# Optimization experiments

Measured on AMD Instinct MI355X. Metric: run time of the kernel, lower is better.

Reference implementation:

```python
import jax, jax.numpy as jnp
import numpy as np

B, SRC_LEN, IN_DIM = 4096, 128, 16
H = 64
SEQ_LEN = 100
MEAN_DIM = 4
COV_DIM = MEAN_DIM + MEAN_DIM * (MEAN_DIM - 1) // 2  # 10
SKIP = 4


def _lin_init(key, out_d, in_d):
    k1, k2 = jax.random.split(key)
    bound = 1.0 / np.sqrt(in_d)
    W = jax.random.uniform(k1, (out_d, in_d), minval=-bound, maxval=bound, dtype=jnp.float32)
    b = jax.random.uniform(k2, (out_d,), minval=-bound, maxval=bound, dtype=jnp.float32)
    return W, b


def setup_inputs() -> dict:
    key = jax.random.key(0)
    ks = jax.random.split(key, 16)
    inp = {}
    inp["x"] = jax.random.normal(ks[0], (B, SRC_LEN, IN_DIM), dtype=jnp.float32)
    inp["trg"] = jax.random.normal(ks[1], (B, 1, SKIP), dtype=jnp.float32)
    # encoder GRU (1 layer)
    inp["enc_Wih"], inp["enc_bih"] = _lin_init(ks[2], 3 * H, IN_DIM)
    inp["enc_Whh"], inp["enc_bhh"] = _lin_init(ks[3], 3 * H, H)
    # decoder GRU (1 layer)
    inp["dec_Wih"], inp["dec_bih"] = _lin_init(ks[4], 3 * H, IN_DIM)
    inp["dec_Whh"], inp["dec_bhh"] = _lin_init(ks[5], 3 * H, H)
    # decoder.out: Linear(H -> IN_DIM)
    inp["out_W"], inp["out_b"] = _lin_init(ks[6], IN_DIM, H)
    # initEmbed: Linear(SKIP -> IN_DIM)
    inp["emb_W"], inp["emb_b"] = _lin_init(ks[7], IN_DIM, SKIP)
    # mean head: Linear(IN_DIM->H), GELU, Linear(H->MEAN_DIM)
    inp["mh_W1"], inp["mh_b1"] = _lin_init(ks[8], H, IN_DIM)
    inp["mh_W2"], inp["mh_b2"] = _lin_init(ks[9], MEAN_DIM, H)
    # cov head: Linear(IN_DIM->H), GELU, Linear(H->COV_DIM)
    inp["ch_W1"], inp["ch_b1"] = _lin_init(ks[10], H, IN_DIM)
    inp["ch_W2"], inp["ch_b2"] = _lin_init(ks[11], COV_DIM, H)
    return inp


def _gru_cell(h, xt, Wih, Whh, bih, bhh):
    # PyTorch GRU cell math. h, xt: [B, H], [B, in]
    gi = xt @ Wih.T + bih           # [B, 3H]
    gh = h @ Whh.T + bhh            # [B, 3H]
    i_r, i_z, i_n = jnp.split(gi, 3, axis=-1)
    h_r, h_z, h_n = jnp.split(gh, 3, axis=-1)
    r = jax.nn.sigmoid(i_r + h_r)
    z = jax.nn.sigmoid(i_z + h_z)
    n = jnp.tanh(i_n + r * h_n)
    return (1.0 - z) * n + z * h


def reference(x, trg, enc_Wih, enc_bih, enc_Whh, enc_bhh,
              dec_Wih, dec_bih, dec_Whh, dec_bhh,
              out_W, out_b, emb_W, emb_b,
              mh_W1, mh_b1, mh_W2, mh_b2,
              ch_W1, ch_b1, ch_W2, ch_b2):
    b = x.shape[0]
    # ---- encoder GRU over src_len; only final hidden is used downstream ----
    h0 = jnp.zeros((b, H), dtype=x.dtype)

    def enc_step(h, xt):
        h = _gru_cell(h, xt, enc_Wih, enc_Whh, enc_bih, enc_bhh)
        return h, None

    enc_h, _ = jax.lax.scan(enc_step, h0, jnp.swapaxes(x, 0, 1))

    init_in = trg[:, 0, :] @ emb_W.T + emb_b  # [B, IN_DIM]

    def dec_step(carry, _):
        h, inp = carry
        h = _gru_cell(h, inp, dec_Wih, dec_Whh, dec_bih, dec_bhh)
        o = h @ out_W.T + out_b               # [B, IN_DIM]
        nxt = jax.lax.stop_gradient(o)        # .detach() on fed-back input
        return (h, nxt), o

    (_, _), outs = jax.lax.scan(dec_step, (enc_h, init_in), None, length=SEQ_LEN)
    dec_out = jnp.swapaxes(outs, 0, 1)        # [B, SEQ_LEN, IN_DIM]

    # ---- output heads (Dropout is identity in eval) ----
    means = jax.nn.gelu(dec_out @ mh_W1.T + mh_b1, approximate=False) @ mh_W2.T + mh_b2
    covs = jax.nn.gelu(dec_out @ ch_W1.T + ch_b1, approximate=False) @ ch_W2.T + ch_b2

    inf = jnp.inf
    lower = jnp.array([-inf, -inf, -1.0, -1.0], dtype=means.dtype)
    upper = jnp.array([inf, inf, 1.0, 1.0], dtype=means.dtype)
    means = jnp.maximum(jnp.minimum(means, upper), lower)
    return means, covs
```

## Files before the change

### kernel.cpp

```cpp
#include <hip/hip_runtime.h>
#include <cstdint>
#include <cstddef>

#define BTOT    4096
#define SRCLEN  128
#define INDIM   16
#define HDIM    64
#define SEQLEN  100
#define MEANS_N (BTOT * SEQLEN * 4)

__device__ __forceinline__ float sigmoidf_(float x) {
    return __builtin_amdgcn_rcpf(1.0f + __expf(-x));
}
__device__ __forceinline__ float tanhf_(float x) {
    float e = __expf(2.0f * x);
    return 1.0f - 2.0f * __builtin_amdgcn_rcpf(e + 1.0f);
}
__device__ __forceinline__ float gelu_fast(float x) {
    float z = fabsf(x) * 0.70710678118654752440f;
    float t = __builtin_amdgcn_rcpf(1.0f + 0.3275911f * z);
    float p = t * (0.254829592f +
              t * (-0.284496736f +
              t * (1.421413741f +
              t * (-1.453152027f +
              t * 1.061405429f))));
    float er = 1.0f - p * __expf(-z * z);
    er = copysignf(er, x);
    return 0.5f * x * (1.0f + er);
}

typedef __attribute__((ext_vector_type(8))) short s8v;
typedef __attribute__((ext_vector_type(4))) float f4v;

__device__ __forceinline__ unsigned short f2bf(float x) {
    unsigned u = __float_as_uint(x);
    unsigned r = (u + 0x7FFFu + ((u >> 16) & 1u)) >> 16;
    return (unsigned short)r;
}
__device__ __forceinline__ float bf2f(unsigned short b) {
    return __uint_as_float(((unsigned)b) << 16);
}
__device__ __forceinline__ void split2(float4 a, float4 b, s8v& hi, s8v& lo) {
    float v[8] = {a.x, a.y, a.z, a.w, b.x, b.y, b.z, b.w};
    #pragma unroll
    for (int j = 0; j < 8; ++j) {
        unsigned short h = f2bf(v[j]);
        hi[j] = (short)h;
        lo[j] = (short)f2bf(v[j] - bf2f(h));
    }
}
__device__ __forceinline__ void split8(const float* v, s8v& hi, s8v& lo) {
    #pragma unroll
    for (int j = 0; j < 8; ++j) {
        unsigned short h = f2bf(v[j]);
        hi[j] = (short)h;
        lo[j] = (short)f2bf(v[j] - bf2f(h));
    }
}
__device__ __forceinline__ void load_bfrag(const float* p, s8v& hi, s8v& lo) {
    float4 a = *(const float4*)p;
    float4 b = *(const float4*)(p + 4);
    split2(a, b, hi, lo);
}

typedef __attribute__((ext_vector_type(2))) unsigned int u2v;
__device__ __forceinline__ float half_merge(float own_lo, float send_hi) {
    u2v r = __builtin_amdgcn_permlane32_swap(__float_as_uint(own_lo),
                                             __float_as_uint(send_hi),
                                             false, false);
    return __uint_as_float(r[0]);
}

#define MFMA16(a, b, c) __builtin_amdgcn_mfma_f32_16x16x32_bf16((a), (b), (c), 0, 0, 0)

__global__ __launch_bounds__(256, 2) void enc_mfma_kernel(
    const float* __restrict__ x,
    const float* __restrict__ Wih, const float* __restrict__ bih,
    const float* __restrict__ Whh, const float* __restrict__ bhh,
    float* __restrict__ enc_h)
{
    const int tid  = threadIdx.x;
    const int lane = tid & 63;
    const int w    = tid >> 6;
    const int col  = lane & 15;
    const int q    = lane >> 4;
    const int u    = w * 16 + col;
    const int b0   = blockIdx.x * 8;
    const int rj0  = (q & 1) * 4 + ((q >> 1) << 1);

    __shared__ __align__(16) unsigned short hiL[2][16][72];
    __shared__ __align__(16) unsigned short loL[2][16][72];
    __shared__ __align__(16) unsigned short xhi_l[64][9][16];
    __shared__ __align__(16) unsigned short xlo_l[64][9][16];

    for (int i = tid; i < 2 * 16 * 72; i += 256) {
        ((unsigned short*)hiL)[i] = 0;
        ((unsigned short*)loL)[i] = 0;
    }
    for (int i = tid; i < 64 * 16; i += 256) {
        xhi_l[i >> 4][8][i & 15] = 0;
        xlo_l[i >> 4][8][i & 15] = 0;
    }

    auto stage_x = [&](int c) {
        #pragma unroll
        for (int k = 0; k < 8; ++k) {
            int f   = tid + k * 256;
            int b   = f >> 8;
            int rem = f & 255;
            int tl  = rem >> 2;
            int d4  = (rem & 3) << 2;
            const float* xp = x + ((size_t)(b0 + b) * SRCLEN + (c * 64 + tl)) * INDIM + d4;
            float4 v = *(const float4*)xp;
            float vv[4] = {v.x, v.y, v.z, v.w};
            unsigned short hh[4], ll[4];
            #pragma unroll
            for (int j = 0; j < 4; ++j) {
                hh[j] = f2bf(vv[j]);
                ll[j] = f2bf(vv[j] - bf2f(hh[j]));
            }
            *(ushort4*)&xhi_l[tl][b][d4] = make_ushort4(hh[0], hh[1], hh[2], hh[3]);
            *(ushort4*)&xlo_l[tl][b][d4] = make_ushort4(ll[0], ll[1], ll[2], ll[3]);
        }
    };

    const s8v z8 = {0, 0, 0, 0, 0, 0, 0, 0};
    const f4v z4 = {0.0f, 0.0f, 0.0f, 0.0f};

    s8v brh[3], brl[3], bzh[3], bzl[3], bnhh[2], bnhl[2], bnxh, bnxl;
    load_bfrag(Whh + (size_t)u * 64 + q * 8,              brh[0], brl[0]);
    load_bfrag(Whh + (size_t)u * 64 + 32 + q * 8,         brh[1], brl[1]);
    load_bfrag(Whh + (size_t)(64 + u) * 64 + q * 8,       bzh[0], bzl[0]);
    load_bfrag(Whh + (size_t)(64 + u) * 64 + 32 + q * 8,  bzh[1], bzl[1]);
    load_bfrag(Whh + (size_t)(128 + u) * 64 + q * 8,      bnhh[0], bnhl[0]);
    load_bfrag(Whh + (size_t)(128 + u) * 64 + 32 + q * 8, bnhh[1], bnhl[1]);
    if (q < 2) {
        load_bfrag(Wih + (size_t)u * 16 + q * 8,         brh[2], brl[2]);
        load_bfrag(Wih + (size_t)(64 + u) * 16 + q * 8,  bzh[2], bzl[2]);
        load_bfrag(Wih + (size_t)(128 + u) * 16 + q * 8, bnxh, bnxl);
    } else {
        brh[2] = z8; brl[2] = z8; bzh[2] = z8; bzl[2] = z8; bnxh = z8; bnxl = z8;
    }

    const float br   = bih[u] + bhh[u];
    const float bz   = bih[u + 64] + bhh[u + 64];
    const float bnx  = bih[u + 128];
    const float bnh  = bhh[u + 128];

    const int xb   = (q < 2) ? (col & 7) : 8;
    const int xoff = (q & 1) * 8;
    const unsigned short* xh_base = &xhi_l[0][xb][xoff];
    const unsigned short* xl_base = &xlo_l[0][xb][xoff];

    stage_x(0);
    float hold2[2] = {0.0f, 0.0f};
    __syncthreads();

    int cur = 0;
    for (int t = 0; t < SRCLEN; ++t) {
        if (t == 64) {
            stage_x(1);
            __syncthreads();
        }
        const int tl = t & 63;

        const s8v xh = *(const s8v*)(xh_base + (size_t)tl * 144);
        const s8v xl = *(const s8v*)(xl_base + (size_t)tl * 144);

        const s8v ah0 = *(const s8v*)&hiL[cur][col][q * 8];
        const s8v al0 = *(const s8v*)&loL[cur][col][q * 8];
        const s8v ah1 = *(const s8v*)&hiL[cur][col][32 + q * 8];
        const s8v al1 = *(const s8v*)&loL[cur][col][32 + q * 8];

        f4v accr, accz, accnh, accnx;
        accr  = MFMA16(ah0, brh[0], z4);
        accz  = MFMA16(ah0, bzh[0], z4);
        accnh = MFMA16(ah0, bnhh[0], z4);
        accr  = MFMA16(ah0, brl[0], accr);
        accz  = MFMA16(ah0, bzl[0], accz);
        accnh = MFMA16(ah0, bnhl[0], accnh);
        accr  = MFMA16(al0, brh[0], accr);
        accz  = MFMA16(al0, bzh[0], accz);
        accnh = MFMA16(al0, bnhh[0], accnh);
        accr  = MFMA16(ah1, brh[1], accr);
        accz  = MFMA16(ah1, bzh[1], accz);
        accnh = MFMA16(ah1, bnhh[1], accnh);
        accr  = MFMA16(ah1, brl[1], accr);
        accz  = MFMA16(ah1, bzl[1], accz);
        accnh = MFMA16(ah1, bnhl[1], accnh);
        accr  = MFMA16(al1, brh[1], accr);
        accz  = MFMA16(al1, bzh[1], accz);
        accnh = MFMA16(al1, bnhh[1], accnh);
        accr  = MFMA16(xh, brh[2], accr);
        accz  = MFMA16(xh, bzh[2], accz);
        accnx = MFMA16(xh, bnxh, z4);
        accr  = MFMA16(xh, brl[2], accr);
        accz  = MFMA16(xh, bzl[2], accz);
        accnx = MFMA16(xh, bnxl, accnx);
        accr  = MFMA16(xl, brh[2], accr);
        accz  = MFMA16(xl, bzh[2], accz);
        accnx = MFMA16(xl, bnxh, accnx);

        float pr[2], pz[2], pnh[2], pnx[2];
        pr[0]  = half_merge(accr[0],  accr[2]);
        pr[1]  = half_merge(accr[1],  accr[3]);
        pz[0]  = half_merge(accz[0],  accz[2]);
        pz[1]  = half_merge(accz[1],  accz[3]);
        pnh[0] = half_merge(accnh[0], accnh[2]);
        pnh[1] = half_merge(accnh[1], accnh[3]);
        pnx[0] = half_merge(accnx[0], accnx[2]);
        pnx[1] = half_merge(accnx[1], accnx[3]);

        const int nxt = cur ^ 1;
        #pragma unroll
        for (int j = 0; j < 2; ++j) {
            float r  = sigmoidf_(pr[j] + br);
            float zz = sigmoidf_(pz[j] + bz);
            float n  = tanhf_(pnx[j] + bnx + r * (pnh[j] + bnh));
            float h  = (1.0f - zz) * n + zz * hold2[j];
            hold2[j] = h;
            unsigned short hh = f2bf(h);
            hiL[nxt][rj0 + j][u] = hh;
            loL[nxt][rj0 + j][u] = f2bf(h - bf2f(hh));
        }
        __syncthreads();
        cur ^= 1;
    }

    enc_h[(size_t)(b0 + rj0) * HDIM + u]     = hold2[0];
    enc_h[(size_t)(b0 + rj0 + 1) * HDIM + u] = hold2[1];
}

__global__ __launch_bounds__(256, 2) void dec_mfma_kernel(
    const float* __restrict__ trg,
    const float* __restrict__ Wih, const float* __restrict__ bih,
    const float* __restrict__ Whh, const float* __restrict__ bhh,
    const float* __restrict__ outW, const float* __restrict__ outb,
    const float* __restrict__ embW, const float* __restrict__ embb,
    const float* __restrict__ enc_h,
    float* __restrict__ dec_o)
{
    const int tid  = threadIdx.x;
    const int lane = tid & 63;
    const int w    = tid >> 6;
    const int col  = lane & 15;
    const int q    = lane >> 4;
    const int u    = w * 16 + col;
    const int b0   = blockIdx.x * 8;
    const int rj0  = (q & 1) * 4 + ((q >> 1) << 1);

    __shared__ __align__(16) unsigned short hiL[2][16][72];
    __shared__ __align__(16) unsigned short loL[2][16][72];
    __shared__ float outW_l[16][64];
    __shared__ float init_l[8][16];

    for (int i = tid; i < 16 * 64; i += 256) outW_l[i >> 6][i & 63] = outW[i];
    if (tid < 128) {
        int b = tid >> 4, jj = tid & 15;
        float s = embb[jj];
        #pragma unroll
        for (int s4 = 0; s4 < 4; ++s4)
            s = fmaf(embW[jj * 4 + s4], trg[(size_t)(b0 + b) * 4 + s4], s);
        init_l[b][jj] = s;
    }
    for (int i = tid; i < 2 * 8 * 72; i += 256) {
        int buf = i / (8 * 72);
        int rr  = (i / 72) & 7;
        int cc  = i % 72;
        hiL[buf][8 + rr][cc] = 0;
        loL[buf][8 + rr][cc] = 0;
    }
    if (tid < 128) {
        int idx = tid * 4;
        int bb = idx >> 6, uu = idx & 63;
        float4 v = *(const float4*)(enc_h + (size_t)(b0 + bb) * HDIM + uu);
        float vv[4] = {v.x, v.y, v.z, v.w};
        #pragma unroll
        for (int j = 0; j < 4; ++j) {
            unsigned short hh = f2bf(vv[j]);
            hiL[0][bb][uu + j] = hh;
            loL[0][bb][uu + j] = f2bf(vv[j] - bf2f(hh));
        }
    }
    float hold2[2];
    hold2[0] = enc_h[(size_t)(b0 + rj0) * HDIM + u];
    hold2[1] = enc_h[(size_t)(b0 + rj0 + 1) * HDIM + u];

    __syncthreads();

    const f4v z4 = {0.0f, 0.0f, 0.0f, 0.0f};

    float wh_r[16], wh_z[16], wh_n[16];
    #pragma unroll
    for (int c = 0; c < 2; ++c)
        #pragma unroll
        for (int jj = 0; jj < 8; ++jj) {
            int k = c * 32 + q * 8 + jj;
            wh_r[c * 8 + jj] = Whh[(size_t)u * 64 + k];
            wh_z[c * 8 + jj] = Whh[(size_t)(64 + u) * 64 + k];
            wh_n[c * 8 + jj] = Whh[(size_t)(128 + u) * 64 + k];
        }
    float wi_r[16], wi_z[16], wi_n[16];
    #pragma unroll
    for (int j = 0; j < 16; ++j) {
        wi_r[j] = Wih[(size_t)u * 16 + j];
        wi_z[j] = Wih[(size_t)(64 + u) * 16 + j];
        wi_n[j] = Wih[(size_t)(128 + u) * 16 + j];
    }

    float m_r[16], m_z[16], c_in[16];
    #pragma unroll
    for (int c = 0; c < 2; ++c)
        #pragma unroll
        for (int jj = 0; jj < 8; ++jj) {
            int k = c * 32 + q * 8 + jj;
            float sr = 0.0f, sz = 0.0f, sn = 0.0f;
            #pragma unroll
            for (int j = 0; j < 16; ++j) {
                float ow = outW_l[j][k];
                sr = fmaf(wi_r[j], ow, sr);
                sz = fmaf(wi_z[j], ow, sz);
                sn = fmaf(wi_n[j], ow, sn);
            }
            m_r[c * 8 + jj]  = wh_r[c * 8 + jj] + sr;
            m_z[c * 8 + jj]  = wh_z[c * 8 + jj] + sz;
            c_in[c * 8 + jj] = sn;
        }

    s8v mrh[2], mrl[2], mzh[2], mzl[2], cinh[2], cinl[2], hnh[2], hnl[2];
    split8(m_r,      mrh[0],  mrl[0]);  split8(m_r + 8,  mrh[1],  mrl[1]);
    split8(m_z,      mzh[0],  mzl[0]);  split8(m_z + 8,  mzh[1],  mzl[1]);
    split8(c_in,     cinh[0], cinl[0]); split8(c_in + 8, cinh[1], cinl[1]);
    split8(wh_n,     hnh[0],  hnl[0]);  split8(wh_n + 8, hnh[1],  hnl[1]);
    s8v r0h[2], r0l[2], z0h[2], z0l[2];
    split8(wh_r, r0h[0], r0l[0]); split8(wh_r + 8, r0h[1], r0l[1]);
    split8(wh_z, z0h[0], z0l[0]); split8(wh_z + 8, z0h[1], z0l[1]);
    s8v owh[2], owl[2];
    {
        float ov[16];
        #pragma unroll
        for (int c = 0; c < 2; ++c)
            #pragma unroll
            for (int jj = 0; jj < 8; ++jj)
                ov[c * 8 + jj] = outW_l[col][c * 32 + q * 8 + jj];
        split8(ov, owh[0], owl[0]); split8(ov + 8, owh[1], owl[1]);
    }

    float b_r = bhh[u] + bih[u];
    float b_z = bhh[u + 64] + bih[u + 64];
    float b_in = bih[u + 128];
    const float b_hn = bhh[u + 128];
    #pragma unroll
    for (int j = 0; j < 16; ++j) {
        float obj = outb[j];
        b_r  = fmaf(obj, wi_r[j], b_r);
        b_z  = fmaf(obj, wi_z[j], b_z);
        b_in = fmaf(obj, wi_n[j], b_in);
    }
    const float ob = outb[col];

    float g_r[2], g_z[2], g_n[2];
    #pragma unroll
    for (int j2 = 0; j2 < 2; ++j2) {
        int row = rj0 + j2;
        float sr = bih[u] + bhh[u];
        float sz = bih[u + 64] + bhh[u + 64];
        float sn = bih[u + 128];
        #pragma unroll
        for (int j = 0; j < 16; ++j) {
            float iv = init_l[row][j];
            sr = fmaf(wi_r[j], iv, sr);
            sz = fmaf(wi_z[j], iv, sz);
            sn = fmaf(wi_n[j], iv, sn);
        }
        g_r[j2] = sr; g_z[j2] = sz; g_n[j2] = sn;
    }

    {
        const s8v ah0 = *(const s8v*)&hiL[0][col][q * 8];
        const s8v al0 = *(const s8v*)&loL[0][col][q * 8];
        const s8v ah1 = *(const s8v*)&hiL[0][col][32 + q * 8];
        const s8v al1 = *(const s8v*)&loL[0][col][32 + q * 8];
        f4v ar, az, ahn;
        ar  = MFMA16(ah0, r0h[0], z4);
        az  = MFMA16(ah0, z0h[0], z4);
        ahn = MFMA16(ah0, hnh[0], z4);
        ar  = MFMA16(ah0, r0l[0], ar);
        az  = MFMA16(ah0, z0l[0], az);
        ahn = MFMA16(ah0, hnl[0], ahn);
        ar  = MFMA16(al0, r0h[0], ar);
        az  = MFMA16(al0, z0h[0], az);
        ahn = MFMA16(al0, hnh[0], ahn);
        ar  = MFMA16(ah1, r0h[1], ar);
        az  = MFMA16(ah1, z0h[1], az);
        ahn = MFMA16(ah1, hnh[1], ahn);
        ar  = MFMA16(ah1, r0l[1], ar);
        az  = MFMA16(ah1, z0l[1], az);
        ahn = MFMA16(ah1, hnl[1], ahn);
        ar  = MFMA16(al1, r0h[1], ar);
        az  = MFMA16(al1, z0h[1], az);
        ahn = MFMA16(al1, hnh[1], ahn);

        float pr[2], pz[2], pnh[2];
        pr[0]  = half_merge(ar[0],  ar[2]);
        pr[1]  = half_merge(ar[1],  ar[3]);
        pz[0]  = half_merge(az[0],  az[2]);
        pz[1]  = half_merge(az[1],  az[3]);
        pnh[0] = half_merge(ahn[0], ahn[2]);
        pnh[1] = half_merge(ahn[1], ahn[3]);

        #pragma unroll
        for (int j = 0; j < 2; ++j) {
            float r  = sigmoidf_(pr[j] + g_r[j]);
            float zz = sigmoidf_(pz[j] + g_z[j]);
            float n  = tanhf_(g_n[j] + r * (pnh[j] + b_hn));
            float h  = (1.0f - zz) * n + zz * hold2[j];
            hold2[j] = h;
            unsigned short hh = f2bf(h);
            hiL[1][rj0 + j][u] = hh;
            loL[1][rj0 + j][u] = f2bf(h - bf2f(hh));
        }
        __syncthreads();
    }

    for (int t = 1; t < SEQLEN; ++t) {
        const int cur = t & 1;
        const s8v ah0 = *(const s8v*)&hiL[cur][col][q * 8];
        const s8v al0 = *(const s8v*)&loL[cur][col][q * 8];
        const s8v ah1 = *(const s8v*)&hiL[cur][col][32 + q * 8];
        const s8v al1 = *(const s8v*)&loL[cur][col][32 + q * 8];

        if (w == ((t - 1) & 3)) {
            f4v oa;
            oa = MFMA16(ah0, owh[0], z4);
            oa = MFMA16(ah0, owl[0], oa);
            oa = MFMA16(al0, owh[0], oa);
            oa = MFMA16(ah1, owh[1], oa);
            oa = MFMA16(ah1, owl[1], oa);
            oa = MFMA16(al1, owh[1], oa);
            if (q < 2) {
                #pragma unroll
                for (int i = 0; i < 4; ++i)
                    dec_o[(((size_t)(b0 + q * 4 + i) * SEQLEN) + (t - 1)) * INDIM + col] = oa[i] + ob;
            }
        }

        f4v ar, az, ain, ahn;
        ar  = MFMA16(ah0, mrh[0], z4);
        az  = MFMA16(ah0, mzh[0], z4);
        ain = MFMA16(ah0, cinh[0], z4);
        ahn = MFMA16(ah0, hnh[0], z4);
        ar  = MFMA16(ah0, mrl[0], ar);
        az  = MFMA16(ah0, mzl[0], az);
        ain = MFMA16(ah0, cinl[0], ain);
        ahn = MFMA16(ah0, hnl[0], ahn);
        ar  = MFMA16(al0, mrh[0], ar);
        az  = MFMA16(al0, mzh[0], az);
        ain = MFMA16(al0, cinh[0], ain);
        ahn = MFMA16(al0, hnh[0], ahn);
        ar  = MFMA16(ah1, mrh[1], ar);
        az  = MFMA16(ah1, mzh[1], az);
        ain = MFMA16(ah1, cinh[1], ain);
        ahn = MFMA16(ah1, hnh[1], ahn);
        ar  = MFMA16(ah1, mrl[1], ar);
        az  = MFMA16(ah1, mzl[1], az);
        ain = MFMA16(ah1, cinl[1], ain);
        ahn = MFMA16(ah1, hnl[1], ahn);
        ar  = MFMA16(al1, mrh[1], ar);
        az  = MFMA16(al1, mzh[1], az);
        ain = MFMA16(al1, cinh[1], ain);
        ahn = MFMA16(al1, hnh[1], ahn);

        float pr[2], pz[2], pin[2], pnh[2];
        pr[0]  = half_merge(ar[0],  ar[2]);
        pr[1]  = half_merge(ar[1],  ar[3]);
        pz[0]  = half_merge(az[0],  az[2]);
        pz[1]  = half_merge(az[1],  az[3]);
        pin[0] = half_merge(ain[0], ain[2]);
        pin[1] = half_merge(ain[1], ain[3]);
        pnh[0] = half_merge(ahn[0], ahn[2]);
        pnh[1] = half_merge(ahn[1], ahn[3]);

        const int nxt = cur ^ 1;
        #pragma unroll
        for (int j = 0; j < 2; ++j) {
            float r  = sigmoidf_(pr[j] + b_r);
            float zz = sigmoidf_(pz[j] + b_z);
            float n  = tanhf_(pin[j] + b_in + r * (pnh[j] + b_hn));
            float h  = (1.0f - zz) * n + zz * hold2[j];
            hold2[j] = h;
            unsigned short hh = f2bf(h);
            hiL[nxt][rj0 + j][u] = hh;
            loL[nxt][rj0 + j][u] = f2bf(h - bf2f(hh));
        }
        __syncthreads();
    }

    if (w == 0) {
        const s8v ah0 = *(const s8v*)&hiL[0][col][q * 8];
        const s8v al0 = *(const s8v*)&loL[0][col][q * 8];
        const s8v ah1 = *(const s8v*)&hiL[0][col][32 + q * 8];
        const s8v al1 = *(const s8v*)&loL[0][col][32 + q * 8];
        f4v oa;
        oa = MFMA16(ah0, owh[0], z4);
        oa = MFMA16(ah0, owl[0], oa);
        oa = MFMA16(al0, owh[0], oa);
        oa = MFMA16(ah1, owh[1], oa);
        oa = MFMA16(ah1, owl[1], oa);
        oa = MFMA16(al1, owh[1], oa);
        if (q < 2) {
            #pragma unroll
            for (int i = 0; i < 4; ++i)
                dec_o[(((size_t)(b0 + q * 4 + i) * SEQLEN) + (SEQLEN - 1)) * INDIM + col] = oa[i] + ob;
        }
    }
}

__global__ __launch_bounds__(256) void heads_kernel(
    const float* __restrict__ dec_o,
    const float* __restrict__ mW1, const float* __restrict__ mb1,
    const float* __restrict__ mW2, const float* __restrict__ mb2,
    const float* __restrict__ cW1, const float* __restrict__ cb1,
    const float* __restrict__ cW2, const float* __restrict__ cb2,
    float* __restrict__ out)
{
    const int tid = threadIdx.x;

    __shared__ __align__(16) float lW1m[64][16];
    __shared__ __align__(16) float lW1c[64][16];
    __shared__ __align__(16) float lW2t[64][16];

    for (int i = tid; i < 1024; i += 256) {
        lW1m[i >> 4][i & 15] = mW1[i];
        lW1c[i >> 4][i & 15] = cW1[i];
    }
    if (tid < 64) {
        #pragma unroll
        for (int j = 0; j < 4; ++j)  lW2t[tid][j]     = mW2[j * 64 + tid];
        #pragma unroll
        for (int j = 0; j < 10; ++j) lW2t[tid][4 + j] = cW2[j * 64 + tid];
        lW2t[tid][14] = mb1[tid];
        lW2t[tid][15] = cb1[tid];
    }
    __syncthreads();

    const size_t rbase = (size_t)blockIdx.x * 1024 + tid;

    float o[4][16];
    #pragma unroll
    for (int k = 0; k < 4; ++k) {
        const float4* op = (const float4*)(dec_o + (rbase + (size_t)k * 256) * 16);
        #pragma unroll
        for (int c = 0; c < 4; ++c) {
            float4 v = op[c];
            o[k][4 * c + 0] = v.x; o[k][4 * c + 1] = v.y;
            o[k][4 * c + 2] = v.z; o[k][4 * c + 3] = v.w;
        }
    }

    float m[4][4], cv[4][10];
    {
        float mb2v[4], cb2v[10];
        #pragma unroll
        for (int j = 0; j < 4; ++j)  mb2v[j] = mb2[j];
        #pragma unroll
        for (int j = 0; j < 10; ++j) cb2v[j] = cb2[j];
        #pragma unroll
        for (int k = 0; k < 4; ++k) {
            #pragma unroll
            for (int j = 0; j < 4; ++j)  m[k][j]  = mb2v[j];
            #pragma unroll
            for (int j = 0; j < 10; ++j) cv[k][j] = cb2v[j];
        }
    }

    #pragma unroll 2
    for (int hu = 0; hu < 64; ++hu) {
        const float4 a0 = *(const float4*)&lW1m[hu][0];
        const float4 a1 = *(const float4*)&lW1m[hu][4];
        const float4 a2 = *(const float4*)&lW1m[hu][8];
        const float4 a3 = *(const float4*)&lW1m[hu][12];
        const float4 c0 = *(const float4*)&lW1c[hu][0];
        const float4 c1 = *(const float4*)&lW1c[hu][4];
        const float4 c2 = *(const float4*)&lW1c[hu][8];
        const float4 c3 = *(const float4*)&lW1c[hu][12];
        const float4 t0 = *(const float4*)&lW2t[hu][0];
        const float4 t1 = *(const float4*)&lW2t[hu][4];
        const float4 t2 = *(const float4*)&lW2t[hu][8];
        const float4 t3 = *(const float4*)&lW2t[hu][12];

        #pragma unroll
        for (int k = 0; k < 4; ++k) {
            float hm = t3.z;
            hm = fmaf(a0.x, o[k][0],  hm); hm = fmaf(a0.y, o[k][1],  hm);
            hm = fmaf(a0.z, o[k][2],  hm); hm = fmaf(a0.w, o[k][3],  hm);
            hm = fmaf(a1.x, o[k][4],  hm); hm = fmaf(a1.y, o[k][5],  hm);
            hm = fmaf(a1.z, o[k][6],  hm); hm = fmaf(a1.w, o[k][7],  hm);
            hm = fmaf(a2.x, o[k][8],  hm); hm = fmaf(a2.y, o[k][9],  hm);
            hm = fmaf(a2.z, o[k][10], hm); hm = fmaf(a2.w, o[k][11], hm);
            hm = fmaf(a3.x, o[k][12], hm); hm = fmaf(a3.y, o[k][13], hm);
            hm = fmaf(a3.z, o[k][14], hm); hm = fmaf(a3.w, o[k][15], hm);
            float gm = gelu_fast(hm);
            m[k][0] = fmaf(t0.x, gm, m[k][0]); m[k][1] = fmaf(t0.y, gm, m[k][1]);
            m[k][2] = fmaf(t0.z, gm, m[k][2]); m[k][3] = fmaf(t0.w, gm, m[k][3]);

            float hc = t3.w;
            hc = fmaf(c0.x, o[k][0],  hc); hc = fmaf(c0.y, o[k][1],  hc);
            hc = fmaf(c0.z, o[k][2],  hc); hc = fmaf(c0.w, o[k][3],  hc);
            hc = fmaf(c1.x, o[k][4],  hc); hc = fmaf(c1.y, o[k][5],  hc);
            hc = fmaf(c1.z, o[k][6],  hc); hc = fmaf(c1.w, o[k][7],  hc);
            hc = fmaf(c2.x, o[k][8],  hc); hc = fmaf(c2.y, o[k][9],  hc);
            hc = fmaf(c2.z, o[k][10], hc); hc = fmaf(c2.w, o[k][11], hc);
            hc = fmaf(c3.x, o[k][12], hc); hc = fmaf(c3.y, o[k][13], hc);
            hc = fmaf(c3.z, o[k][14], hc); hc = fmaf(c3.w, o[k][15], hc);
            float gc = gelu_fast(hc);
            cv[k][0] = fmaf(t1.x, gc, cv[k][0]); cv[k][1] = fmaf(t1.y, gc, cv[k][1]);
            cv[k][2] = fmaf(t1.z, gc, cv[k][2]); cv[k][3] = fmaf(t1.w, gc, cv[k][3]);
            cv[k][4] = fmaf(t2.x, gc, cv[k][4]); cv[k][5] = fmaf(t2.y, gc, cv[k][5]);
            cv[k][6] = fmaf(t2.z, gc, cv[k][6]); cv[k][7] = fmaf(t2.w, gc, cv[k][7]);
            cv[k][8] = fmaf(t3.x, gc, cv[k][8]); cv[k][9] = fmaf(t3.y, gc, cv[k][9]);
        }
    }

    float* means = out;
    float* covs  = out + MEANS_N;
    #pragma unroll
    for (int k = 0; k < 4; ++k) {
        const size_t r = rbase + (size_t)k * 256;
        m[k][2] = fminf(fmaxf(m[k][2], -1.0f), 1.0f);
        m[k][3] = fminf(fmaxf(m[k][3], -1.0f), 1.0f);
        #pragma unroll
        for (int j = 0; j < 4; ++j)  means[r * 4 + j] = m[k][j];
        #pragma unroll
        for (int j = 0; j < 10; ++j) covs[r * 10 + j] = cv[k][j];
    }
}

extern "C" void kernel_launch(void* const* d_in, const int* in_sizes, int n_in,
                              void* d_out, int out_size, void* d_ws, size_t ws_size,
                              hipStream_t stream)
{
    const float* x    = (const float*)d_in[0];
    const float* trg  = (const float*)d_in[1];
    const float* eWih = (const float*)d_in[2];
    const float* ebih = (const float*)d_in[3];
    const float* eWhh = (const float*)d_in[4];
    const float* ebhh = (const float*)d_in[5];
    const float* dWih = (const float*)d_in[6];
    const float* dbih = (const float*)d_in[7];
    const float* dWhh = (const float*)d_in[8];
    const float* dbhh = (const float*)d_in[9];
    const float* outW = (const float*)d_in[10];
    const float* outb = (const float*)d_in[11];
    const float* embW = (const float*)d_in[12];
    const float* embb = (const float*)d_in[13];
    const float* mW1  = (const float*)d_in[14];
    const float* mb1  = (const float*)d_in[15];
    const float* mW2  = (const float*)d_in[16];
    const float* mb2  = (const float*)d_in[17];
    const float* cW1  = (const float*)d_in[18];
    const float* cb1  = (const float*)d_in[19];
    const float* cW2  = (const float*)d_in[20];
    const float* cb2  = (const float*)d_in[21];

    float* ws    = (float*)d_ws;
    float* enc_h = ws;
    float* dec_o = ws + (size_t)BTOT * HDIM;
    float* outp  = (float*)d_out;

    enc_mfma_kernel<<<dim3(BTOT / 8), dim3(256), 0, stream>>>(x, eWih, ebih, eWhh, ebhh, enc_h);
    dec_mfma_kernel<<<dim3(BTOT / 8), dim3(256), 0, stream>>>(trg, dWih, dbih, dWhh, dbhh,
                                                              outW, outb, embW, embb, enc_h, dec_o);
    heads_kernel<<<dim3((BTOT * SEQLEN) / 1024), dim3(256), 0, stream>>>(
        dec_o, mW1, mb1, mW2, mb2, cW1, cb1, cW2, cb2, outp);
}
```

Baseline: 374.8 us.

## Fuse encoder and decoder GRU kernels and halve rows per heads thread

Merges the encoder and decoder GRU kernels into one kernel, so the encoder's final hidden state passes directly in registers and LDS instead of through a global workspace round-trip and a second launch. The decoder weight setup now follows the encoder loop in the same block. The heads kernel is also changed to process 2 rows per thread instead of 4, doubling its grid. The trade-offs are higher register and LDS pressure in the fused kernel, which could reduce occupancy, and less per-thread reuse of head weights.

```diff
diff --git a/kernel.cpp b/kernel.cpp
--- a/kernel.cpp
+++ b/kernel.cpp
@@ -73,11 +73,16 @@
 
 #define MFMA16(a, b, c) __builtin_amdgcn_mfma_f32_16x16x32_bf16((a), (b), (c), 0, 0, 0)
 
-__global__ __launch_bounds__(256, 2) void enc_mfma_kernel(
+__global__ __launch_bounds__(256, 2) void fused_gru_kernel(
     const float* __restrict__ x,
-    const float* __restrict__ Wih, const float* __restrict__ bih,
-    const float* __restrict__ Whh, const float* __restrict__ bhh,
-    float* __restrict__ enc_h)
+    const float* __restrict__ eWih, const float* __restrict__ ebih,
+    const float* __restrict__ eWhh, const float* __restrict__ ebhh,
+    const float* __restrict__ dWih, const float* __restrict__ dbih,
+    const float* __restrict__ dWhh, const float* __restrict__ dbhh,
+    const float* __restrict__ outW, const float* __restrict__ outb,
+    const float* __restrict__ embW, const float* __restrict__ embb,
+    const float* __restrict__ trg,
+    float* __restrict__ dec_o)
 {
     const int tid  = threadIdx.x;
     const int lane = tid & 63;
@@ -92,6 +97,18 @@
     __shared__ __align__(16) unsigned short loL[2][16][72];
     __shared__ __align__(16) unsigned short xhi_l[64][9][16];
     __shared__ __align__(16) unsigned short xlo_l[64][9][16];
+    __shared__ float outW_l[16][64];
+    __shared__ float init_l[8][16];
+
+    for (int i = tid; i < 16 * 64; i += 256) outW_l[i >> 6][i & 63] = outW[i];
+    if (tid < 128) {
+        int b = tid >> 4, jj = tid & 15;
+        float s = embb[jj];
+        #pragma unroll
+        for (int s4 = 0; s4 < 4; ++s4)
+            s = fmaf(embW[jj * 4 + s4], trg[(size_t)(b0 + b) * 4 + s4], s);
+        init_l[b][jj] = s;
+    }
 
     for (int i = tid; i < 2 * 16 * 72; i += 256) {
         ((unsigned short*)hiL)[i] = 0;
@@ -127,310 +144,320 @@
     const s8v z8 = {0, 0, 0, 0, 0, 0, 0, 0};
     const f4v z4 = {0.0f, 0.0f, 0.0f, 0.0f};
 
-    s8v brh[3], brl[3], bzh[3], bzl[3], bnhh[2], bnhl[2], bnxh, bnxl;
-    load_bfrag(Whh + (size_t)u * 64 + q * 8,              brh[0], brl[0]);
-    load_bfrag(Whh + (size_t)u * 64 + 32 + q * 8,         brh[1], brl[1]);
-    load_bfrag(Whh + (size_t)(64 + u) * 64 + q * 8,       bzh[0], bzl[0]);
-    load_bfrag(Whh + (size_t)(64 + u) * 64 + 32 + q * 8,  bzh[1], bzl[1]);
-    load_bfrag(Whh + (size_t)(128 + u) * 64 + q * 8,      bnhh[0], bnhl[0]);
-    load_bfrag(Whh + (size_t)(128 + u) * 64 + 32 + q * 8, bnhh[1], bnhl[1]);
-    if (q < 2) {
-        load_bfrag(Wih + (size_t)u * 16 + q * 8,         brh[2], brl[2]);
-        load_bfrag(Wih + (size_t)(64 + u) * 16 + q * 8,  bzh[2], bzl[2]);
-        load_bfrag(Wih + (size_t)(128 + u) * 16 + q * 8, bnxh, bnxl);
-    } else {
-        brh[2] = z8; brl[2] = z8; bzh[2] = z8; bzl[2] = z8; bnxh = z8; bnxl = z8;
-    }
-
-    const float br   = bih[u] + bhh[u];
-    const float bz   = bih[u + 64] + bhh[u + 64];
-    const float bnx  = bih[u + 128];
-    const float bnh  = bhh[u + 128];
-
-    const int xb   = (q < 2) ? (col & 7) : 8;
-    const int xoff = (q & 1) * 8;
-    const unsigned short* xh_base = &xhi_l[0][xb][xoff];
-    const unsigned short* xl_base = &xlo_l[0][xb][xoff];
-
-    stage_x(0);
-    float hold2[2] = {0.0f, 0.0f};
-    __syncthreads();
-
-    int cur = 0;
-    for (int t = 0; t < SRCLEN; ++t) {
-        if (t == 64) {
-            stage_x(1);
+    {
+        s8v brh[3], brl[3], bzh[3], bzl[3], bnhh[2], bnhl[2], bnxh, bnxl;
+        load_bfrag(eWhh + (size_t)u * 64 + q * 8,              brh[0], brl[0]);
+        load_bfrag(eWhh + (size_t)u * 64 + 32 + q * 8,         brh[1], brl[1]);
+        load_bfrag(eWhh + (size_t)(64 + u) * 64 + q * 8,       bzh[0], bzl[0]);
+        load_bfrag(eWhh + (size_t)(64 + u) * 64 + 32 + q * 8,  bzh[1], bzl[1]);
+        load_bfrag(eWhh + (size_t)(128 + u) * 64 + q * 8,      bnhh[0], bnhl[0]);
+        load_bfrag(eWhh + (size_t)(128 + u) * 64 + 32 + q * 8, bnhh[1], bnhl[1]);
+        if (q < 2) {
+            load_bfrag(eWih + (size_t)u * 16 + q * 8,         brh[2], brl[2]);
+            load_bfrag(eWih + (size_t)(64 + u) * 16 + q * 8,  bzh[2], bzl[2]);
+            load_bfrag(eWih + (size_t)(128 + u) * 16 + q * 8, bnxh, bnxl);
+        } else {
+            brh[2] = z8; brl[2] = z8; bzh[2] = z8; bzl[2] = z8; bnxh = z8; bnxl = z8;
+        }
+
+        const float br   = ebih[u] + ebhh[u];
+        const float bz   = ebih[u + 64] + ebhh[u + 64];
+        const float bnx  = ebih[u + 128];
+        const float bnh  = ebhh[u + 128];
+
+        const int xb   = (q < 2) ? (col & 7) : 8;
+        const int xoff = (q & 1) * 8;
+        const unsigned short* xh_base = &xhi_l[0][xb][xoff];
+        const unsigned short* xl_base = &xlo_l[0][xb][xoff];
+
+        stage_x(0);
+        float hold2e[2] = {0.0f, 0.0f};
+        __syncthreads();
+
+        int cur = 0;
+        for (int t = 0; t < SRCLEN; ++t) {
+            if (t == 64) {
+                stage_x(1);
+                __syncthreads();
+            }
+            const int tl = t & 63;
+
+            const s8v xh = *(const s8v*)(xh_base + (size_t)tl * 144);
+            const s8v xl = *(const s8v*)(xl_base + (size_t)tl * 144);
+
+            const s8v ah0 = *(const s8v*)&hiL[cur][col][q * 8];
+            const s8v al0 = *(const s8v*)&loL[cur][col][q * 8];
+            const s8v ah1 = *(const s8v*)&hiL[cur][col][32 + q * 8];
+            const s8v al1 = *(const s8v*)&loL[cur][col][32 + q * 8];
+
+            f4v accr, accz, accnh, accnx;
+            accr  = MFMA16(ah0, brh[0], z4);
+            accz  = MFMA16(ah0, bzh[0], z4);
+            accnh = MFMA16(ah0, bnhh[0], z4);
+            accr  = MFMA16(ah0, brl[0], accr);
+            accz  = MFMA16(ah0, bzl[0], accz);
+            accnh = MFMA16(ah0, bnhl[0], accnh);
+            accr  = MFMA16(al0, brh[0], accr);
+            accz  = MFMA16(al0, bzh[0], accz);
+            accnh = MFMA16(al0, bnhh[0], accnh);
+            accr  = MFMA16(ah1, brh[1], accr);
+            accz  = MFMA16(ah1, bzh[1], accz);
+            accnh = MFMA16(ah1, bnhh[1], accnh);
+            accr  = MFMA16(ah1, brl[1], accr);
+            accz  = MFMA16(ah1, bzl[1], accz);
+            accnh = MFMA16(ah1, bnhl[1], accnh);
+            accr  = MFMA16(al1, brh[1], accr);
+            accz  = MFMA16(al1, bzh[1], accz);
+            accnh = MFMA16(al1, bnhh[1], accnh);
+            accr  = MFMA16(xh, brh[2], accr);
+            accz  = MFMA16(xh, bzh[2], accz);
+            accnx = MFMA16(xh, bnxh, z4);
+            accr  = MFMA16(xh, brl[2], accr);
+            accz  = MFMA16(xh, bzl[2], accz);
+            accnx = MFMA16(xh, bnxl, accnx);
+            accr  = MFMA16(xl, brh[2], accr);
+            accz  = MFMA16(xl, bzh[2], accz);
+            accnx = MFMA16(xl, bnxh, accnx);
+
+            float pr[2], pz[2], pnh[2], pnx[2];
+            pr[0]  = half_merge(accr[0],  accr[2]);
+            pr[1]  = half_merge(accr[1],  accr[3]);
+            pz[0]  = half_merge(accz[0],  accz[2]);
+            pz[1]  = half_merge(accz[1],  accz[3]);
+            pnh[0] = half_merge(accnh[0], accnh[2]);
+            pnh[1] = half_merge(accnh[1], accnh[3]);
+            pnx[0] = half_merge(accnx[0], accnx[2]);
+            pnx[1] = half_merge(accnx[1], accnx[3]);
+
+            const int nxt = cur ^ 1;
+            #pragma unroll
+            for (int j = 0; j < 2; ++j) {
+                float r  = sigmoidf_(pr[j] + br);
+                float zz = sigmoidf_(pz[j] + bz);
+                float n  = tanhf_(pnx[j] + bnx + r * (pnh[j] + bnh));
+                float h  = (1.0f - zz) * n + zz * hold2e[j];
+                hold2e[j] = h;
+                unsigned short hh = f2bf(h);
+                hiL[nxt][rj0 + j][u] = hh;
+                loL[nxt][rj0 + j][u] = f2bf(h - bf2f(hh));
+            }
             __syncthreads();
-        }
-        const int tl = t & 63;
-
-        const s8v xh = *(const s8v*)(xh_base + (size_t)tl * 144);
-        const s8v xl = *(const s8v*)(xl_base + (size_t)tl * 144);
-
-        const s8v ah0 = *(const s8v*)&hiL[cur][col][q * 8];
-        const s8v al0 = *(const s8v*)&loL[cur][col][q * 8];
-        const s8v ah1 = *(const s8v*)&hiL[cur][col][32 + q * 8];
-        const s8v al1 = *(const s8v*)&loL[cur][col][32 + q * 8];
-
-        f4v accr, accz, accnh, accnx;
-        accr  = MFMA16(ah0, brh[0], z4);
-        accz  = MFMA16(ah0, bzh[0], z4);
-        accnh = MFMA16(ah0, bnhh[0], z4);
-        accr  = MFMA16(ah0, brl[0], accr);
-        accz  = MFMA16(ah0, bzl[0], accz);
-        accnh = MFMA16(ah0, bnhl[0], accnh);
-        accr  = MFMA16(al0, brh[0], accr);
-        accz  = MFMA16(al0, bzh[0], accz);
-        accnh = MFMA16(al0, bnhh[0], accnh);
-        accr  = MFMA16(ah1, brh[1], accr);
-        accz  = MFMA16(ah1, bzh[1], accz);
-        accnh = MFMA16(ah1, bnhh[1], accnh);
-        accr  = MFMA16(ah1, brl[1], accr);
-        accz  = MFMA16(ah1, bzl[1], accz);
-        accnh = MFMA16(ah1, bnhl[1], accnh);
-        accr  = MFMA16(al1, brh[1], accr);
-        accz  = MFMA16(al1, bzh[1], accz);
-        accnh = MFMA16(al1, bnhh[1], accnh);
-        accr  = MFMA16(xh, brh[2], accr);
-        accz  = MFMA16(xh, bzh[2], accz);
-        accnx = MFMA16(xh, bnxh, z4);
-        accr  = MFMA16(xh, brl[2], accr);
-        accz  = MFMA16(xh, bzl[2], accz);
-        accnx = MFMA16(xh, bnxl, accnx);
-        accr  = MFMA16(xl, brh[2], accr);
-        accz  = MFMA16(xl, bzh[2], accz);
-        accnx = MFMA16(xl, bnxh, accnx);
-
-        float pr[2], pz[2], pnh[2], pnx[2];
-        pr[0]  = half_merge(accr[0],  accr[2]);
-        pr[1]  = half_merge(accr[1],  accr[3]);
-        pz[0]  = half_merge(accz[0],  accz[2]);
-        pz[1]  = half_merge(accz[1],  accz[3]);
-        pnh[0] = half_merge(accnh[0], accnh[2]);
-        pnh[1] = half_merge(accnh[1], accnh[3]);
-        pnx[0] = half_merge(accnx[0], accnx[2]);
-        pnx[1] = half_merge(accnx[1], accnx[3]);
-
-        const int nxt = cur ^ 1;
-        #pragma unroll
-        for (int j = 0; j < 2; ++j) {
-            float r  = sigmoidf_(pr[j] + br);
-            float zz = sigmoidf_(pz[j] + bz);
-            float n  = tanhf_(pnx[j] + bnx + r * (pnh[j] + bnh));
-            float h  = (1.0f - zz) * n + zz * hold2[j];
-            hold2[j] = h;
-            unsigned short hh = f2bf(h);
-            hiL[nxt][rj0 + j][u] = hh;
-            loL[nxt][rj0 + j][u] = f2bf(h - bf2f(hh));
-        }
-        __syncthreads();
-        cur ^= 1;
-    }
-
-    enc_h[(size_t)(b0 + rj0) * HDIM + u]     = hold2[0];
-    enc_h[(size_t)(b0 + rj0 + 1) * HDIM + u] = hold2[1];
-}
-
-__global__ __launch_bounds__(256, 2) void dec_mfma_kernel(
-    const float* __restrict__ trg,
-    const float* __restrict__ Wih, const float* __restrict__ bih,
-    const float* __restrict__ Whh, const float* __restrict__ bhh,
-    const float* __restrict__ outW, const float* __restrict__ outb,
-    const float* __restrict__ embW, const float* __restrict__ embb,
-    const float* __restrict__ enc_h,
-    float* __restrict__ dec_o)
-{
-    const int tid  = threadIdx.x;
-    const int lane = tid & 63;
-    const int w    = tid >> 6;
-    const int col  = lane & 15;
-    const int q    = lane >> 4;
-    const int u    = w * 16 + col;
-    const int b0   = blockIdx.x * 8;
-    const int rj0  = (q & 1) * 4 + ((q >> 1) << 1);
-
-    __shared__ __align__(16) unsigned short hiL[2][16][72];
-    __shared__ __align__(16) unsigned short loL[2][16][72];
-    __shared__ float outW_l[16][64];
-    __shared__ float init_l[8][16];
-
-    for (int i = tid; i < 16 * 64; i += 256) outW_l[i >> 6][i & 63] = outW[i];
-    if (tid < 128) {
-        int b = tid >> 4, jj = tid & 15;
-        float s = embb[jj];
-        #pragma unroll
-        for (int s4 = 0; s4 < 4; ++s4)
-            s = fmaf(embW[jj * 4 + s4], trg[(size_t)(b0 + b) * 4 + s4], s);
-        init_l[b][jj] = s;
-    }
-    for (int i = tid; i < 2 * 8 * 72; i += 256) {
-        int buf = i / (8 * 72);
-        int rr  = (i / 72) & 7;
-        int cc  = i % 72;
-        hiL[buf][8 + rr][cc] = 0;
-        loL[buf][8 + rr][cc] = 0;
-    }
-    if (tid < 128) {
-        int idx = tid * 4;
-        int bb = idx >> 6, uu = idx & 63;
-        float4 v = *(const float4*)(enc_h + (size_t)(b0 + bb) * HDIM + uu);
-        float vv[4] = {v.x, v.y, v.z, v.w};
-        #pragma unroll
-        for (int j = 0; j < 4; ++j) {
-            unsigned short hh = f2bf(vv[j]);
-            hiL[0][bb][uu + j] = hh;
-            loL[0][bb][uu + j] = f2bf(vv[j] - bf2f(hh));
-        }
-    }
-    float hold2[2];
-    hold2[0] = enc_h[(size_t)(b0 + rj0) * HDIM + u];
-    hold2[1] = enc_h[(size_t)(b0 + rj0 + 1) * HDIM + u];
-
-    __syncthreads();
-
-    const f4v z4 = {0.0f, 0.0f, 0.0f, 0.0f};
-
-    float wh_r[16], wh_z[16], wh_n[16];
-    #pragma unroll
-    for (int c = 0; c < 2; ++c)
-        #pragma unroll
-        for (int jj = 0; jj < 8; ++jj) {
-            int k = c * 32 + q * 8 + jj;
-            wh_r[c * 8 + jj] = Whh[(size_t)u * 64 + k];
-            wh_z[c * 8 + jj] = Whh[(size_t)(64 + u) * 64 + k];
-            wh_n[c * 8 + jj] = Whh[(size_t)(128 + u) * 64 + k];
-        }
-    float wi_r[16], wi_z[16], wi_n[16];
-    #pragma unroll
-    for (int j = 0; j < 16; ++j) {
-        wi_r[j] = Wih[(size_t)u * 16 + j];
-        wi_z[j] = Wih[(size_t)(64 + u) * 16 + j];
-        wi_n[j] = Wih[(size_t)(128 + u) * 16 + j];
-    }
-
-    float m_r[16], m_z[16], c_in[16];
-    #pragma unroll
-    for (int c = 0; c < 2; ++c)
-        #pragma unroll
-        for (int jj = 0; jj < 8; ++jj) {
-            int k = c * 32 + q * 8 + jj;
-            float sr = 0.0f, sz = 0.0f, sn = 0.0f;
+            cur ^= 1;
+        }
+
+        float hold2[2] = {hold2e[0], hold2e[1]};
+
+        float wh_r[16], wh_z[16], wh_n[16];
+        #pragma unroll
+        for (int c = 0; c < 2; ++c)
+            #pragma unroll
+            for (int jj = 0; jj < 8; ++jj) {
+                int k = c * 32 + q * 8 + jj;
+                wh_r[c * 8 + jj] = dWhh[(size_t)u * 64 + k];
+                wh_z[c * 8 + jj] = dWhh[(size_t)(64 + u) * 64 + k];
+                wh_n[c * 8 + jj] = dWhh[(size_t)(128 + u) * 64 + k];
+            }
+        float wi_r[16], wi_z[16], wi_n[16];
+        #pragma unroll
+        for (int j = 0; j < 16; ++j) {
+            wi_r[j] = dWih[(size_t)u * 16 + j];
+            wi_z[j] = dWih[(size_t)(64 + u) * 16 + j];
+            wi_n[j] = dWih[(size_t)(128 + u) * 16 + j];
+        }
+
+        float m_r[16], m_z[16], c_in[16];
+        #pragma unroll
+        for (int c = 0; c < 2; ++c)
+            #pragma unroll
+            for (int jj = 0; jj < 8; ++jj) {
+                int k = c * 32 + q * 8 + jj;
+                float sr = 0.0f, sz = 0.0f, sn = 0.0f;
+                #pragma unroll
+                for (int j = 0; j < 16; ++j) {
+                    float ow = outW_l[j][k];
+                    sr = fmaf(wi_r[j], ow, sr);
+                    sz = fmaf(wi_z[j], ow, sz);
+                    sn = fmaf(wi_n[j], ow, sn);
+                }
+                m_r[c * 8 + jj]  = wh_r[c * 8 + jj] + sr;
+                m_z[c * 8 + jj]  = wh_z[c * 8 + jj] + sz;
+                c_in[c * 8 + jj] = sn;
+            }
+
+        s8v mrh[2], mrl[2], mzh[2], mzl[2], cinh[2], cinl[2], hnh[2], hnl[2];
+        split8(m_r,      mrh[0],  mrl[0]);  split8(m_r + 8,  mrh[1],  mrl[1]);
+        split8(m_z,      mzh[0],  mzl[0]);  split8(m_z + 8,  mzh[1],  mzl[1]);
+        split8(c_in,     cinh[0], cinl[0]); split8(c_in + 8, cinh[1], cinl[1]);
+        split8(wh_n,     hnh[0],  hnl[0]);  split8(wh_n + 8, hnh[1],  hnl[1]);
+        s8v r0h[2], r0l[2], z0h[2], z0l[2];
+        split8(wh_r, r0h[0], r0l[0]); split8(wh_r + 8, r0h[1], r0l[1]);
+        split8(wh_z, z0h[0], z0l[0]); split8(wh_z + 8, z0h[1], z0l[1]);
+        s8v owh[2], owl[2];
+        {
+            float ov[16];
+            #pragma unroll
+            for (int c = 0; c < 2; ++c)
+                #pragma unroll
+                for (int jj = 0; jj < 8; ++jj)
+                    ov[c * 8 + jj] = outW_l[col][c * 32 + q * 8 + jj];
+            split8(ov, owh[0], owl[0]); split8(ov + 8, owh[1], owl[1]);
+        }
+
+        float b_r = dbhh[u] + dbih[u];
+        float b_z = dbhh[u + 64] + dbih[u + 64];
+        float b_in = dbih[u + 128];
+        const float b_hn = dbhh[u + 128];
+        #pragma unroll
+        for (int j = 0; j < 16; ++j) {
+            float obj = outb[j];
+            b_r  = fmaf(obj, wi_r[j], b_r);
+            b_z  = fmaf(obj, wi_z[j], b_z);
+            b_in = fmaf(obj, wi_n[j], b_in);
+        }
+        const float ob = outb[col];
+
+        float g_r[2], g_z[2], g_n[2];
+        #pragma unroll
+        for (int j2 = 0; j2 < 2; ++j2) {
+            int row = rj0 + j2;
+            float sr = dbih[u] + dbhh[u];
+            float sz = dbih[u + 64] + dbhh[u + 64];
+            float sn = dbih[u + 128];
             #pragma unroll
             for (int j = 0; j < 16; ++j) {
-                float ow = outW_l[j][k];
-                sr = fmaf(wi_r[j], ow, sr);
-                sz = fmaf(wi_z[j], ow, sz);
-                sn = fmaf(wi_n[j], ow, sn);
-            }
-            m_r[c * 8 + jj]  = wh_r[c * 8 + jj] + sr;
-            m_z[c * 8 + jj]  = wh_z[c * 8 + jj] + sz;
-            c_in[c * 8 + jj] = sn;
-        }
-
-    s8v mrh[2], mrl[2], mzh[2], mzl[2], cinh[2], cinl[2], hnh[2], hnl[2];
-    split8(m_r,      mrh[0],  mrl[0]);  split8(m_r + 8,  mrh[1],  mrl[1]);
-    split8(m_z,      mzh[0],  mzl[0]);  split8(m_z + 8,  mzh[1],  mzl[1]);
-    split8(c_in,     cinh[0], cinl[0]); split8(c_in + 8, cinh[1], cinl[1]);
-    split8(wh_n,     hnh[0],  hnl[0]);  split8(wh_n + 8, hnh[1],  hnl[1]);
-    s8v r0h[2], r0l[2], z0h[2], z0l[2];
-    split8(wh_r, r0h[0], r0l[0]); split8(wh_r + 8, r0h[1], r0l[1]);
-    split8(wh_z, z0h[0], z0l[0]); split8(wh_z + 8, z0h[1], z0l[1]);
-    s8v owh[2], owl[2];
-    {
-        float ov[16];
-        #pragma unroll
-        for (int c = 0; c < 2; ++c)
-            #pragma unroll
-            for (int jj = 0; jj < 8; ++jj)
-                ov[c * 8 + jj] = outW_l[col][c * 32 + q * 8 + jj];
-        split8(ov, owh[0], owl[0]); split8(ov + 8, owh[1], owl[1]);
-    }
-
-    float b_r = bhh[u] + bih[u];
-    float b_z = bhh[u + 64] + bih[u + 64];
-    float b_in = bih[u + 128];
-    const float b_hn = bhh[u + 128];
-    #pragma unroll
-    for (int j = 0; j < 16; ++j) {
-        float obj = outb[j];
-        b_r  = fmaf(obj, wi_r[j], b_r);
-        b_z  = fmaf(obj, wi_z[j], b_z);
-        b_in = fmaf(obj, wi_n[j], b_in);
-    }
-    const float ob = outb[col];
-
-    float g_r[2], g_z[2], g_n[2];
-    #pragma unroll
-    for (int j2 = 0; j2 < 2; ++j2) {
-        int row = rj0 + j2;
-        float sr = bih[u] + bhh[u];
-        float sz = bih[u + 64] + bhh[u + 64];
-        float sn = bih[u + 128];
-        #pragma unroll
-        for (int j = 0; j < 16; ++j) {
-            float iv = init_l[row][j];
-            sr = fmaf(wi_r[j], iv, sr);
-            sz = fmaf(wi_z[j], iv, sz);
-            sn = fmaf(wi_n[j], iv, sn);
-        }
-        g_r[j2] = sr; g_z[j2] = sz; g_n[j2] = sn;
-    }
-
-    {
-        const s8v ah0 = *(const s8v*)&hiL[0][col][q * 8];
-        const s8v al0 = *(const s8v*)&loL[0][col][q * 8];
-        const s8v ah1 = *(const s8v*)&hiL[0][col][32 + q * 8];
-        const s8v al1 = *(const s8v*)&loL[0][col][32 + q * 8];
-        f4v ar, az, ahn;
-        ar  = MFMA16(ah0, r0h[0], z4);
-        az  = MFMA16(ah0, z0h[0], z4);
-        ahn = MFMA16(ah0, hnh[0], z4);
-        ar  = MFMA16(ah0, r0l[0], ar);
-        az  = MFMA16(ah0, z0l[0], az);
-        ahn = MFMA16(ah0, hnl[0], ahn);
-        ar  = MFMA16(al0, r0h[0], ar);
-        az  = MFMA16(al0, z0h[0], az);
-        ahn = MFMA16(al0, hnh[0], ahn);
-        ar  = MFMA16(ah1, r0h[1], ar);
-        az  = MFMA16(ah1, z0h[1], az);
-        ahn = MFMA16(ah1, hnh[1], ahn);
-        ar  = MFMA16(ah1, r0l[1], ar);
-        az  = MFMA16(ah1, z0l[1], az);
-        ahn = MFMA16(ah1, hnl[1], ahn);
-        ar  = MFMA16(al1, r0h[1], ar);
-        az  = MFMA16(al1, z0h[1], az);
-        ahn = MFMA16(al1, hnh[1], ahn);
-
-        float pr[2], pz[2], pnh[2];
-        pr[0]  = half_merge(ar[0],  ar[2]);
-        pr[1]  = half_merge(ar[1],  ar[3]);
-        pz[0]  = half_merge(az[0],  az[2]);
-        pz[1]  = half_merge(az[1],  az[3]);
-        pnh[0] = half_merge(ahn[0], ahn[2]);
-        pnh[1] = half_merge(ahn[1], ahn[3]);
-
-        #pragma unroll
-        for (int j = 0; j < 2; ++j) {
-            float r  = sigmoidf_(pr[j] + g_r[j]);
-            float zz = sigmoidf_(pz[j] + g_z[j]);
-            float n  = tanhf_(g_n[j] + r * (pnh[j] + b_hn));
-            float h  = (1.0f - zz) * n + zz * hold2[j];
-            hold2[j] = h;
-            unsigned short hh = f2bf(h);
-            hiL[1][rj0 + j][u] = hh;
-            loL[1][rj0 + j][u] = f2bf(h - bf2f(hh));
-        }
-        __syncthreads();
-    }
-
-    for (int t = 1; t < SEQLEN; ++t) {
-        const int cur = t & 1;
-        const s8v ah0 = *(const s8v*)&hiL[cur][col][q * 8];
-        const s8v al0 = *(const s8v*)&loL[cur][col][q * 8];
-        const s8v ah1 = *(const s8v*)&hiL[cur][col][32 + q * 8];
-        const s8v al1 = *(const s8v*)&loL[cur][col][32 + q * 8];
-
-        if (w == ((t - 1) & 3)) {
+                float iv = init_l[row][j];
+                sr = fmaf(wi_r[j], iv, sr);
+                sz = fmaf(wi_z[j], iv, sz);
+                sn = fmaf(wi_n[j], iv, sn);
+            }
+            g_r[j2] = sr; g_z[j2] = sz; g_n[j2] = sn;
+        }
+
+        {
+            const s8v ah0 = *(const s8v*)&hiL[0][col][q * 8];
+            const s8v al0 = *(const s8v*)&loL[0][col][q * 8];
+            const s8v ah1 = *(const s8v*)&hiL[0][col][32 + q * 8];
+            const s8v al1 = *(const s8v*)&loL[0][col][32 + q * 8];
+            f4v ar, az, ahn;
+            ar  = MFMA16(ah0, r0h[0], z4);
+            az  = MFMA16(ah0, z0h[0], z4);
+            ahn = MFMA16(ah0, hnh[0], z4);
+            ar  = MFMA16(ah0, r0l[0], ar);
+            az  = MFMA16(ah0, z0l[0], az);
+            ahn = MFMA16(ah0, hnl[0], ahn);
+            ar  = MFMA16(al0, r0h[0], ar);
+            az  = MFMA16(al0, z0h[0], az);
+            ahn = MFMA16(al0, hnh[0], ahn);
+            ar  = MFMA16(ah1, r0h[1], ar);
+            az  = MFMA16(ah1, z0h[1], az);
+            ahn = MFMA16(ah1, hnh[1], ahn);
+            ar  = MFMA16(ah1, r0l[1], ar);
+            az  = MFMA16(ah1, z0l[1], az);
+            ahn = MFMA16(ah1, hnl[1], ahn);
+            ar  = MFMA16(al1, r0h[1], ar);
+            az  = MFMA16(al1, z0h[1], az);
+            ahn = MFMA16(al1, hnh[1], ahn);
+
+            float pr[2], pz[2], pnh[2];
+            pr[0]  = half_merge(ar[0],  ar[2]);
+            pr[1]  = half_merge(ar[1],  ar[3]);
+            pz[0]  = half_merge(az[0],  az[2]);
+            pz[1]  = half_merge(az[1],  az[3]);
+            pnh[0] = half_merge(ahn[0], ahn[2]);
+            pnh[1] = half_merge(ahn[1], ahn[3]);
+
+            #pragma unroll
+            for (int j = 0; j < 2; ++j) {
+                float r  = sigmoidf_(pr[j] + g_r[j]);
+                float zz = sigmoidf_(pz[j] + g_z[j]);
+                float n  = tanhf_(g_n[j] + r * (pnh[j] + b_hn));
+                float h  = (1.0f - zz) * n + zz * hold2[j];
+                hold2[j] = h;
+                unsigned short hh = f2bf(h);
+                hiL[1][rj0 + j][u] = hh;
+                loL[1][rj0 + j][u] = f2bf(h - bf2f(hh));
+            }
+            __syncthreads();
+        }
+
+        for (int t = 1; t < SEQLEN; ++t) {
+            const int dcur = t & 1;
+            const s8v ah0 = *(const s8v*)&hiL[dcur][col][q * 8];
+            const s8v al0 = *(const s8v*)&loL[dcur][col][q * 8];
+            const s8v ah1 = *(const s8v*)&hiL[dcur][col][32 + q * 8];
+            const s8v al1 = *(const s8v*)&loL[dcur][col][32 + q * 8];
+
+            if (w == ((t - 1) & 3)) {
+                f4v oa;
+                oa = MFMA16(ah0, owh[0], z4);
+                oa = MFMA16(ah0, owl[0], oa);
+                oa = MFMA16(al0, owh[0], oa);
+                oa = MFMA16(ah1, owh[1], oa);
+                oa = MFMA16(ah1, owl[1], oa);
+                oa = MFMA16(al1, owh[1], oa);
+                if (q < 2) {
+                    #pragma unroll
+                    for (int i = 0; i < 4; ++i)
+                        dec_o[(((size_t)(b0 + q * 4 + i) * SEQLEN) + (t - 1)) * INDIM + col] = oa[i] + ob;
+                }
+            }
+
+            f4v ar, az, ain, ahn;
+            ar  = MFMA16(ah0, mrh[0], z4);
+            az  = MFMA16(ah0, mzh[0], z4);
+            ain = MFMA16(ah0, cinh[0], z4);
+            ahn = MFMA16(ah0, hnh[0], z4);
+            ar  = MFMA16(ah0, mrl[0], ar);
+            az  = MFMA16(ah0, mzl[0], az);
+            ain = MFMA16(ah0, cinl[0], ain);
+            ahn = MFMA16(ah0, hnl[0], ahn);
+            ar  = MFMA16(al0, mrh[0], ar);
+            az  = MFMA16(al0, mzh[0], az);
+            ain = MFMA16(al0, cinh[0], ain);
+            ahn = MFMA16(al0, hnh[0], ahn);
+            ar  = MFMA16(ah1, mrh[1], ar);
+            az  = MFMA16(ah1, mzh[1], az);
+            ain = MFMA16(ah1, cinh[1], ain);
+            ahn = MFMA16(ah1, hnh[1], ahn);
+            ar  = MFMA16(ah1, mrl[1], ar);
+            az  = MFMA16(ah1, mzl[1], az);
+            ain = MFMA16(ah1, cinl[1], ain);
+            ahn = MFMA16(ah1, hnl[1], ahn);
+            ar  = MFMA16(al1, mrh[1], ar);
+            az  = MFMA16(al1, mzh[1], az);
+            ain = MFMA16(al1, cinh[1], ain);
+            ahn = MFMA16(al1, hnh[1], ahn);
+
+            float pr[2], pz[2], pin[2], pnh[2];
+            pr[0]  = half_merge(ar[0],  ar[2]);
+            pr[1]  = half_merge(ar[1],  ar[3]);
+            pz[0]  = half_merge(az[0],  az[2]);
+            pz[1]  = half_merge(az[1],  az[3]);
+            pin[0] = half_merge(ain[0], ain[2]);
+            pin[1] = half_merge(ain[1], ain[3]);
+            pnh[0] = half_merge(ahn[0], ahn[2]);
+            pnh[1] = half_merge(ahn[1], ahn[3]);
+
+            const int nxt = dcur ^ 1;
+            #pragma unroll
+            for (int j = 0; j < 2; ++j) {
+                float r  = sigmoidf_(pr[j] + b_r);
+                float zz = sigmoidf_(pz[j] + b_z);
+                float n  = tanhf_(pin[j] + b_in + r * (pnh[j] + b_hn));
+                float h  = (1.0f - zz) * n + zz * hold2[j];
+                hold2[j] = h;
+                unsigned short hh = f2bf(h);
+                hiL[nxt][rj0 + j][u] = hh;
+                loL[nxt][rj0 + j][u] = f2bf(h - bf2f(hh));
+            }
+            __syncthreads();
+        }
+
+        if (w == 0) {
+            const s8v ah0 = *(const s8v*)&hiL[0][col][q * 8];
+            const s8v al0 = *(const s8v*)&loL[0][col][q * 8];
+            const s8v ah1 = *(const s8v*)&hiL[0][col][32 + q * 8];
+            const s8v al1 = *(const s8v*)&loL[0][col][32 + q * 8];
             f4v oa;
             oa = MFMA16(ah0, owh[0], z4);
             oa = MFMA16(ah0, owl[0], oa);
@@ -441,77 +468,8 @@
             if (q < 2) {
                 #pragma unroll
                 for (int i = 0; i < 4; ++i)
-                    dec_o[(((size_t)(b0 + q * 4 + i) * SEQLEN) + (t - 1)) * INDIM + col] = oa[i] + ob;
-            }
-        }
-
-        f4v ar, az, ain, ahn;
-        ar  = MFMA16(ah0, mrh[0], z4);
-        az  = MFMA16(ah0, mzh[0], z4);
-        ain = MFMA16(ah0, cinh[0], z4);
-        ahn = MFMA16(ah0, hnh[0], z4);
-        ar  = MFMA16(ah0, mrl[0], ar);
-        az  = MFMA16(ah0, mzl[0], az);
-        ain = MFMA16(ah0, cinl[0], ain);
-        ahn = MFMA16(ah0, hnl[0], ahn);
-        ar  = MFMA16(al0, mrh[0], ar);
-        az  = MFMA16(al0, mzh[0], az);
-        ain = MFMA16(al0, cinh[0], ain);
-        ahn = MFMA16(al0, hnh[0], ahn);
-        ar  = MFMA16(ah1, mrh[1], ar);
-        az  = MFMA16(ah1, mzh[1], az);
-        ain = MFMA16(ah1, cinh[1], ain);
-        ahn = MFMA16(ah1, hnh[1], ahn);
-        ar  = MFMA16(ah1, mrl[1], ar);
-        az  = MFMA16(ah1, mzl[1], az);
-        ain = MFMA16(ah1, cinl[1], ain);
-        ahn = MFMA16(ah1, hnl[1], ahn);
-        ar  = MFMA16(al1, mrh[1], ar);
-        az  = MFMA16(al1, mzh[1], az);
-        ain = MFMA16(al1, cinh[1], ain);
-        ahn = MFMA16(al1, hnh[1], ahn);
-
-        float pr[2], pz[2], pin[2], pnh[2];
-        pr[0]  = half_merge(ar[0],  ar[2]);
-        pr[1]  = half_merge(ar[1],  ar[3]);
-        pz[0]  = half_merge(az[0],  az[2]);
-        pz[1]  = half_merge(az[1],  az[3]);
-        pin[0] = half_merge(ain[0], ain[2]);
-        pin[1] = half_merge(ain[1], ain[3]);
-        pnh[0] = half_merge(ahn[0], ahn[2]);
-        pnh[1] = half_merge(ahn[1], ahn[3]);
-
-        const int nxt = cur ^ 1;
-        #pragma unroll
-        for (int j = 0; j < 2; ++j) {
-            float r  = sigmoidf_(pr[j] + b_r);
-            float zz = sigmoidf_(pz[j] + b_z);
-            float n  = tanhf_(pin[j] + b_in + r * (pnh[j] + b_hn));
-            float h  = (1.0f - zz) * n + zz * hold2[j];
-            hold2[j] = h;
-            unsigned short hh = f2bf(h);
-            hiL[nxt][rj0 + j][u] = hh;
-            loL[nxt][rj0 + j][u] = f2bf(h - bf2f(hh));
-        }
-        __syncthreads();
-    }
-
-    if (w == 0) {
-        const s8v ah0 = *(const s8v*)&hiL[0][col][q * 8];
-        const s8v al0 = *(const s8v*)&loL[0][col][q * 8];
-        const s8v ah1 = *(const s8v*)&hiL[0][col][32 + q * 8];
-        const s8v al1 = *(const s8v*)&loL[0][col][32 + q * 8];
-        f4v oa;
-        oa = MFMA16(ah0, owh[0], z4);
-        oa = MFMA16(ah0, owl[0], oa);
-        oa = MFMA16(al0, owh[0], oa);
-        oa = MFMA16(ah1, owh[1], oa);
-        oa = MFMA16(ah1, owl[1], oa);
-        oa = MFMA16(al1, owh[1], oa);
-        if (q < 2) {
-            #pragma unroll
-            for (int i = 0; i < 4; ++i)
-                dec_o[(((size_t)(b0 + q * 4 + i) * SEQLEN) + (SEQLEN - 1)) * INDIM + col] = oa[i] + ob;
+                    dec_o[(((size_t)(b0 + q * 4 + i) * SEQLEN) + (SEQLEN - 1)) * INDIM + col] = oa[i] + ob;
+            }
         }
     }
 }
@@ -544,12 +502,12 @@
     }
     __syncthreads();
 
-    const size_t rbase = (size_t)blockIdx.x * 1024 + tid;
-
-    float o[4][16];
+    const size_t r0 = (size_t)blockIdx.x * 512 + tid;
+
+    float o[2][16];
     #pragma unroll
-    for (int k = 0; k < 4; ++k) {
-        const float4* op = (const float4*)(dec_o + (rbase + (size_t)k * 256) * 16);
+    for (int k = 0; k < 2; ++k) {
+        const float4* op = (const float4*)(dec_o + (r0 + (size_t)k * 256) * 16);
         #pragma unroll
         for (int c = 0; c < 4; ++c) {
             float4 v = op[c];
@@ -558,20 +516,13 @@
         }
     }
 
-    float m[4][4], cv[4][10];
-    {
-        float mb2v[4], cb2v[10];
-        #pragma unroll
-        for (int j = 0; j < 4; ++j)  mb2v[j] = mb2[j];
-        #pragma unroll
-        for (int j = 0; j < 10; ++j) cb2v[j] = cb2[j];
-        #pragma unroll
-        for (int k = 0; k < 4; ++k) {
-            #pragma unroll
-            for (int j = 0; j < 4; ++j)  m[k][j]  = mb2v[j];
-            #pragma unroll
-            for (int j = 0; j < 10; ++j) cv[k][j] = cb2v[j];
-        }
+    float m[2][4], cv[2][10];
+    #pragma unroll
+    for (int k = 0; k < 2; ++k) {
+        #pragma unroll
+        for (int j = 0; j < 4; ++j)  m[k][j]  = mb2[j];
+        #pragma unroll
+        for (int j = 0; j < 10; ++j) cv[k][j] = cb2[j];
     }
 
     #pragma unroll 2
@@ -590,7 +541,7 @@
         const float4 t3 = *(const float4*)&lW2t[hu][12];
 
         #pragma unroll
-        for (int k = 0; k < 4; ++k) {
+        for (int k = 0; k < 2; ++k) {
             float hm = t3.z;
             hm = fmaf(a0.x, o[k][0],  hm); hm = fmaf(a0.y, o[k][1],  hm);
             hm = fmaf(a0.z, o[k][2],  hm); hm = fmaf(a0.w, o[k][3],  hm);
@@ -625,8 +576,8 @@
     float* means = out;
     float* covs  = out + MEANS_N;
     #pragma unroll
-    for (int k = 0; k < 4; ++k) {
-        const size_t r = rbase + (size_t)k * 256;
+    for (int k = 0; k < 2; ++k) {
+        const size_t r = r0 + (size_t)k * 256;
         m[k][2] = fminf(fmaxf(m[k][2], -1.0f), 1.0f);
         m[k][3] = fminf(fmaxf(m[k][3], -1.0f), 1.0f);
         #pragma unroll
@@ -664,13 +615,12 @@
     const float* cb2  = (const float*)d_in[21];
 
     float* ws    = (float*)d_ws;
-    float* enc_h = ws;
-    float* dec_o = ws + (size_t)BTOT * HDIM;
+    float* dec_o = ws;
     float* outp  = (float*)d_out;
 
-    enc_mfma_kernel<<<dim3(BTOT / 8), dim3(256), 0, stream>>>(x, eWih, ebih, eWhh, ebhh, enc_h);
-    dec_mfma_kernel<<<dim3(BTOT / 8), dim3(256), 0, stream>>>(trg, dWih, dbih, dWhh, dbhh,
-                                                              outW, outb, embW, embb, enc_h, dec_o);
-    heads_kernel<<<dim3((BTOT * SEQLEN) / 1024), dim3(256), 0, stream>>>(
+    fused_gru_kernel<<<dim3(BTOT / 8), dim3(256), 0, stream>>>(
+        x, eWih, ebih, eWhh, ebhh, dWih, dbih, dWhh, dbhh,
+        outW, outb, embW, embb, trg, dec_o);
+    heads_kernel<<<dim3((BTOT * SEQLEN) / 512), dim3(256), 0, stream>>>(
         dec_o, mW1, mb1, mW2, mb2, cW1, cb1, cW2, cb2, outp);
 }
```

Measured after the change: 358.4 us. 1.05x faster.
